# Kernel tuning notes

Measured on AMD Instinct MI355X. Metric: run time of the kernel, lower is better.

Reference implementation:

```python
import jax, jax.numpy as jnp
import numpy as np

B, H, S, DK = 2, 16, 2048, 64
P_DROP = 0.5
MASK_NEG = 1e9


def setup_inputs() -> dict:
    key = jax.random.key(0)
    kq, kk, kv = jax.random.split(key, 3)
    Q = jax.random.normal(kq, (B, H, S, DK), dtype=jnp.float32)
    K = jax.random.normal(kk, (B, H, S, DK), dtype=jnp.float32)
    V = jax.random.normal(kv, (B, H, S, DK), dtype=jnp.float32)
    attn_mask = jnp.ones((B, 1, S, S), dtype=jnp.float32)  # 1 = attend, 0 = masked
    return {"Q": Q, "K": K, "V": V, "attn_mask": attn_mask}


def reference(Q, K, V, attn_mask):
    # scores = Q @ K^T / sqrt(d_k)
    scores = jnp.einsum('bhqd,bhkd->bhqk', Q, K) / np.float32(np.sqrt(DK))
    # additive mask: (mask - 1) * 1e9
    scores = scores + (attn_mask - 1.0) * MASK_NEG
    attn = jax.nn.softmax(scores, axis=-1)
    # dropout p=0.5 (training mode in the torch module); deterministic key for reproducibility
    keep = jax.random.bernoulli(jax.random.key(42), 1.0 - P_DROP, attn.shape)
    attn_dropped = jnp.where(keep, attn / (1.0 - P_DROP), 0.0)
    context = jnp.einsum('bhqk,bhkd->bhqd', attn_dropped, V)
    return context, attn
```

## Files before the change

kernel.cpp:

```cpp
#include <hip/hip_runtime.h>
#include <stdint.h>

#define B_ 2
#define H_ 16
#define S_ 2048
#define D_ 64

__device__ __forceinline__ unsigned tf_keep(unsigned idx) {
  const unsigned k0 = 0u, k1 = 42u;
  const unsigned ks2 = k0 ^ k1 ^ 0x1BD11BDAu;
  unsigned x0 = k0;
  unsigned x1 = idx + k1;
#define ROTL(v, r) (((v) << (r)) | ((v) >> (32 - (r))))
#define RND(r) { x0 += x1; x1 = ROTL(x1, r); x1 ^= x0; }
  RND(13) RND(15) RND(26) RND(6)
  x0 += k1;  x1 += ks2 + 1u;
  RND(17) RND(29) RND(16) RND(24)
  x0 += ks2; x1 += k0 + 2u;
  RND(13) RND(15) RND(26) RND(6)
  x0 += k0;  x1 += k1 + 3u;
  RND(17) RND(29) RND(16) RND(24)
  x0 += k1;  x1 += ks2 + 4u;
  RND(13) RND(15) RND(26) RND(6)
  x0 += ks2; x1 += k0 + 5u;
#undef RND
#undef ROTL
  return ((x0 ^ x1) >> 31) ^ 1u;
}

extern "C" __global__ void __launch_bounds__(256, 2)
k1_scores(const float* __restrict__ Q, const float* __restrict__ K,
          const float* __restrict__ mask, float* __restrict__ E,
          float* __restrict__ inv_sums) {
  __shared__ float Qs[D_][16];
  __shared__ float Ks[D_][128];
  const int tid = threadIdx.x;
  const int w = tid >> 6, lane = tid & 63;
  const int qt = blockIdx.x & 127, bh = blockIdx.x >> 7, b = bh >> 4;
  const int q0 = qt << 4;

  const float* Qb = Q + ((size_t)bh * S_ + q0) * D_;
  const float* Kb = K + (size_t)bh * S_ * D_;
  const float* Mb = mask + ((size_t)b * S_ + q0) * S_;
  float* Eb = E + ((size_t)bh * S_ + q0) * S_;

  {
    const int ql = tid >> 4, d4 = tid & 15;
    const float4 v = *(const float4*)(Qb + ql * D_ + (d4 << 2));
    Qs[(d4 << 2) + 0][ql] = v.x;
    Qs[(d4 << 2) + 1][ql] = v.y;
    Qs[(d4 << 2) + 2][ql] = v.z;
    Qs[(d4 << 2) + 3][ql] = v.w;
  }

  float row_sum[4] = {0.0f, 0.0f, 0.0f, 0.0f};

  for (int kt = 0; kt < 16; ++kt) {
    __syncthreads();
#pragma unroll
    for (int rep = 0; rep < 8; ++rep) {
      const int item = (rep << 8) + tid;
      const int kl = item & 127, d4 = item >> 7;
      const float4 v = *(const float4*)(Kb + ((size_t)(kt << 7) + kl) * D_ + (d4 << 2));
      Ks[(d4 << 2) + 0][kl] = v.x;
      Ks[(d4 << 2) + 1][kl] = v.y;
      Ks[(d4 << 2) + 2][kl] = v.z;
      Ks[(d4 << 2) + 3][kl] = v.w;
    }
    __syncthreads();

    float sA[4] = {0.f, 0.f, 0.f, 0.f}, sB[4] = {0.f, 0.f, 0.f, 0.f};
#pragma unroll 16
    for (int d = 0; d < D_; ++d) {
      const float4 qv = *(const float4*)&Qs[d][w << 2];
      const float2 kv = *(const float2*)&Ks[d][lane << 1];
      const float qa[4] = {qv.x, qv.y, qv.z, qv.w};
#pragma unroll
      for (int i = 0; i < 4; ++i) {
        sA[i] += qa[i] * kv.x;
        sB[i] += qa[i] * kv.y;
      }
    }

    const int kc = (kt << 7) + (lane << 1);
#pragma unroll
    for (int i = 0; i < 4; ++i) {
      const int row = (w << 2) + i;
      const float2 mv = *(const float2*)(Mb + (size_t)row * S_ + kc);
      const float ex = __expf(sA[i] * 0.125f + (mv.x - 1.0f) * 1e9f);
      const float ey = __expf(sB[i] * 0.125f + (mv.y - 1.0f) * 1e9f);
      row_sum[i] += ex + ey;
      *(float2*)(Eb + (size_t)row * S_ + kc) = make_float2(ex, ey);
    }
  }

#pragma unroll
  for (int i = 0; i < 4; ++i) {
    float v = row_sum[i];
#pragma unroll
    for (int off = 32; off >= 1; off >>= 1) v += __shfl_xor(v, off, 64);
    row_sum[i] = v;
  }
  if (lane < 4) {
    float v = row_sum[0];
    if (lane == 1) v = row_sum[1];
    else if (lane == 2) v = row_sum[2];
    else if (lane == 3) v = row_sum[3];
    inv_sums[(size_t)bh * S_ + q0 + (w << 2) + lane] = 1.0f / v;
  }
}

extern "C" __global__ void __launch_bounds__(256, 2)
k2_pv(const float* __restrict__ V, const float* __restrict__ inv_sums,
      float* __restrict__ E ,
      float* __restrict__ ctx) {
  __shared__ float Vs[64][64];
  __shared__ float Ps[64][68];
  __shared__ float invs[64];
  const int tid = threadIdx.x;
  const int dg = tid & 15, qg = tid >> 4;
  const int qt = blockIdx.x & 31, bh = blockIdx.x >> 5;
  const int q0 = qt << 6;

  const float* Vb = V + (size_t)bh * S_ * D_;
  float* Eb = E + ((size_t)bh * S_ + q0) * S_;

  if (tid < 64) invs[tid] = inv_sums[(size_t)bh * S_ + q0 + tid];

  float acc[4][4];
#pragma unroll
  for (int i = 0; i < 4; ++i)
#pragma unroll
    for (int m = 0; m < 4; ++m) acc[i][m] = 0.0f;

  const unsigned rowbase = (unsigned)bh * S_ + (unsigned)q0;

  for (int kt = 0; kt < 32; ++kt) {
    __syncthreads();
#pragma unroll
    for (int rep = 0; rep < 4; ++rep) {
      const int idx = (rep << 8) + tid;
      const int d4 = idx & 15, kk = idx >> 4;
      const float4 v = *(const float4*)(Vb + ((size_t)(kt << 6) + kk) * D_ + (d4 << 2));
      *(float4*)&Vs[kk][d4 << 2] = v;
    }
#pragma unroll
    for (int rep = 0; rep < 4; ++rep) {
      const int idx = (rep << 8) + tid;
      const int k4 = idx & 15, ql = idx >> 4;
      float* ep = Eb + (size_t)ql * S_ + (kt << 6) + (k4 << 2);
      const float4 e = *(const float4*)ep;
      const float inv = invs[ql];
      const float4 an = make_float4(e.x * inv, e.y * inv, e.z * inv, e.w * inv);
      *(float4*)ep = an;
      const unsigned fb = ((rowbase + (unsigned)ql) << 11) +
                          (unsigned)((kt << 6) + (k4 << 2));
      Ps[(k4 << 2) + 0][ql] = tf_keep(fb + 0u) ? an.x * 2.0f : 0.0f;
      Ps[(k4 << 2) + 1][ql] = tf_keep(fb + 1u) ? an.y * 2.0f : 0.0f;
      Ps[(k4 << 2) + 2][ql] = tf_keep(fb + 2u) ? an.z * 2.0f : 0.0f;
      Ps[(k4 << 2) + 3][ql] = tf_keep(fb + 3u) ? an.w * 2.0f : 0.0f;
    }
    __syncthreads();
#pragma unroll 8
    for (int kk = 0; kk < 64; ++kk) {
      const float4 pq = *(const float4*)&Ps[kk][qg << 2];
      const float4 vv = *(const float4*)&Vs[kk][dg << 2];
      acc[0][0] += pq.x * vv.x; acc[0][1] += pq.x * vv.y; acc[0][2] += pq.x * vv.z; acc[0][3] += pq.x * vv.w;
      acc[1][0] += pq.y * vv.x; acc[1][1] += pq.y * vv.y; acc[1][2] += pq.y * vv.z; acc[1][3] += pq.y * vv.w;
      acc[2][0] += pq.z * vv.x; acc[2][1] += pq.z * vv.y; acc[2][2] += pq.z * vv.z; acc[2][3] += pq.z * vv.w;
      acc[3][0] += pq.w * vv.x; acc[3][1] += pq.w * vv.y; acc[3][2] += pq.w * vv.z; acc[3][3] += pq.w * vv.w;
    }
  }

  float* cb = ctx + ((size_t)bh * S_ + q0 + (qg << 2)) * D_ + (dg << 2);
#pragma unroll
  for (int i = 0; i < 4; ++i) {
    const float4 o = make_float4(acc[i][0], acc[i][1], acc[i][2], acc[i][3]);
    *(float4*)(cb + (size_t)i * D_) = o;
  }
}

extern "C" void kernel_launch(void* const* d_in, const int* in_sizes, int n_in,
                              void* d_out, int out_size, void* d_ws, size_t ws_size,
                              hipStream_t stream) {
  (void)in_sizes; (void)n_in; (void)out_size; (void)ws_size;
  const float* Q = (const float*)d_in[0];
  const float* K = (const float*)d_in[1];
  const float* V = (const float*)d_in[2];
  const float* mask = (const float*)d_in[3];
  float* ctx = (float*)d_out;
  float* attn = ctx + (size_t)B_ * H_ * S_ * D_;
  float* inv_sums = (float*)d_ws;

  hipLaunchKernelGGL(k1_scores, dim3(B_ * H_ * (S_ / 16)), dim3(256), 0, stream,
                     Q, K, mask, attn, inv_sums);
  hipLaunchKernelGGL(k2_pv, dim3(B_ * H_ * (S_ / 64)), dim3(256), 0, stream,
                     V, inv_sums, attn, ctx);
}
```

Measured before the change: 1.351 ms.

## Fuse score, softmax and PV kernels with bf16 exp cache in LDS

Replaces the two-kernel pipeline with a single fused kernel. Each block of 32 queries computes the exponentiated scores and keeps them in shared memory as bf16, computes the dropout-masked P·V product on the fly, and writes normalized attn once at the end. This removes the global round trip of the unnormalized exp matrix (one write, one read and one rewrite) and the second launch. The cost is large LDS usage (about 128KB for the bf16 cache), which limits occupancy, plus bf16 rounding of attn and of the P used for the context, which risks tolerance failures.

Measured after the change: 2.147 ms. +58.8%, slower.

```diff
diff --git a/kernel.cpp b/kernel.cpp
--- a/kernel.cpp
+++ b/kernel.cpp
@@ -5,6 +5,9 @@
 #define H_ 16
 #define S_ 2048
 #define D_ 64
+#define QT 32
+#define KT 64
+#define NKT (S_ / KT)
 
 __device__ __forceinline__ unsigned tf_keep(unsigned idx) {
   const unsigned k0 = 0u, k1 = 42u;
@@ -28,172 +31,203 @@
   return ((x0 ^ x1) >> 31) ^ 1u;
 }
 
-extern "C" __global__ void __launch_bounds__(256, 2)
-k1_scores(const float* __restrict__ Q, const float* __restrict__ K,
-          const float* __restrict__ mask, float* __restrict__ E,
-          float* __restrict__ inv_sums) {
-  __shared__ float Qs[D_][16];
-  __shared__ float Ks[D_][128];
+__device__ __forceinline__ unsigned short bf16_rne(float f) {
+  unsigned u = __float_as_uint(f);
+  u += 0x7fffu + ((u >> 16) & 1u);
+  return (unsigned short)(u >> 16);
+}
+
+__device__ __forceinline__ void unpk(unsigned u, float& lo, float& hi) {
+  lo = __uint_as_float(u << 16);
+  hi = __uint_as_float(u & 0xffff0000u);
+}
+
+extern "C" __global__ void __launch_bounds__(512, 2)
+fused_attn(const float* __restrict__ Q, const float* __restrict__ K,
+           const float* __restrict__ V, const float* __restrict__ mask,
+           float* __restrict__ ctx, float* __restrict__ attn) {
+  __shared__ __align__(16) float Qs[QT][68];
+  __shared__ __align__(16) float KVs[KT][64];
+  __shared__ __align__(16) unsigned short Es[QT][S_];
+  __shared__ __align__(16) unsigned short Pd[QT][72];
+  __shared__ float invs[QT];
+
   const int tid = threadIdx.x;
   const int w = tid >> 6, lane = tid & 63;
-  const int qt = blockIdx.x & 127, bh = blockIdx.x >> 7, b = bh >> 4;
-  const int q0 = qt << 4;
+  const int qt = blockIdx.x & 63;
+  const int bh = blockIdx.x >> 6;
+  const int b = bh >> 4;
+  const int q0 = qt << 5;
 
   const float* Qb = Q + ((size_t)bh * S_ + q0) * D_;
   const float* Kb = K + (size_t)bh * S_ * D_;
+  const float* Vb = V + (size_t)bh * S_ * D_;
   const float* Mb = mask + ((size_t)b * S_ + q0) * S_;
-  float* Eb = E + ((size_t)bh * S_ + q0) * S_;
+  const unsigned rowbase = (unsigned)(bh * S_ + q0);
 
   {
-    const int ql = tid >> 4, d4 = tid & 15;
-    const float4 v = *(const float4*)(Qb + ql * D_ + (d4 << 2));
-    Qs[(d4 << 2) + 0][ql] = v.x;
-    Qs[(d4 << 2) + 1][ql] = v.y;
-    Qs[(d4 << 2) + 2][ql] = v.z;
-    Qs[(d4 << 2) + 3][ql] = v.w;
-  }
-
-  float row_sum[4] = {0.0f, 0.0f, 0.0f, 0.0f};
-
-  for (int kt = 0; kt < 16; ++kt) {
-    __syncthreads();
-#pragma unroll
-    for (int rep = 0; rep < 8; ++rep) {
-      const int item = (rep << 8) + tid;
-      const int kl = item & 127, d4 = item >> 7;
-      const float4 v = *(const float4*)(Kb + ((size_t)(kt << 7) + kl) * D_ + (d4 << 2));
-      Ks[(d4 << 2) + 0][kl] = v.x;
-      Ks[(d4 << 2) + 1][kl] = v.y;
-      Ks[(d4 << 2) + 2][kl] = v.z;
-      Ks[(d4 << 2) + 3][kl] = v.w;
-    }
-    __syncthreads();
-
-    float sA[4] = {0.f, 0.f, 0.f, 0.f}, sB[4] = {0.f, 0.f, 0.f, 0.f};
-#pragma unroll 16
-    for (int d = 0; d < D_; ++d) {
-      const float4 qv = *(const float4*)&Qs[d][w << 2];
-      const float2 kv = *(const float2*)&Ks[d][lane << 1];
-      const float qa[4] = {qv.x, qv.y, qv.z, qv.w};
-#pragma unroll
-      for (int i = 0; i < 4; ++i) {
-        sA[i] += qa[i] * kv.x;
-        sB[i] += qa[i] * kv.y;
-      }
-    }
-
-    const int kc = (kt << 7) + (lane << 1);
+    const int qr = tid >> 4, d4 = tid & 15;
+    const float4 v = *(const float4*)(Qb + (size_t)qr * D_ + (d4 << 2));
+    *(float4*)&Qs[qr][d4 << 2] = v;
+  }
+
+  const int ksp = tid >> 8;
+  const int t8 = tid & 255;
+  const int qg2 = t8 >> 4;
+  const int dg = t8 & 15;
+
+  float rsum[4] = {0.f, 0.f, 0.f, 0.f};
+  float aA[4] = {0.f, 0.f, 0.f, 0.f};
+  float aB[4] = {0.f, 0.f, 0.f, 0.f};
+
+  const int ksw = lane & 15;
+  const float4* krow = (const float4*)&KVs[lane][0];
+
+#pragma unroll 1
+  for (int kt = 0; kt < NKT; ++kt) {
+    __syncthreads();
+#pragma unroll
+    for (int rep = 0; rep < 2; ++rep) {
+      const int f4 = (rep << 9) + tid;
+      const int kr = f4 >> 4, d4 = f4 & 15;
+      const float4 v = *(const float4*)(Kb + (size_t)((kt << 6) + kr) * D_ + (d4 << 2));
+      *(float4*)&KVs[kr][(d4 ^ (kr & 15)) << 2] = v;
+    }
+    __syncthreads();
+
+    const int kg = (kt << 6) + lane;
+    float mv0 = Mb[(size_t)((w << 2) + 0) * S_ + kg];
+    float mv1 = Mb[(size_t)((w << 2) + 1) * S_ + kg];
+    float mv2 = Mb[(size_t)((w << 2) + 2) * S_ + kg];
+    float mv3 = Mb[(size_t)((w << 2) + 3) * S_ + kg];
+
+    float s0 = 0.f, s1 = 0.f, s2 = 0.f, s3 = 0.f;
+#pragma unroll
+    for (int d4 = 0; d4 < 16; ++d4) {
+      const float4 kv = krow[d4 ^ ksw];
+      const float4 q0v = *(const float4*)&Qs[(w << 2) + 0][d4 << 2];
+      const float4 q1v = *(const float4*)&Qs[(w << 2) + 1][d4 << 2];
+      const float4 q2v = *(const float4*)&Qs[(w << 2) + 2][d4 << 2];
+      const float4 q3v = *(const float4*)&Qs[(w << 2) + 3][d4 << 2];
+      s0 = fmaf(q0v.x, kv.x, s0); s0 = fmaf(q0v.y, kv.y, s0);
+      s0 = fmaf(q0v.z, kv.z, s0); s0 = fmaf(q0v.w, kv.w, s0);
+      s1 = fmaf(q1v.x, kv.x, s1); s1 = fmaf(q1v.y, kv.y, s1);
+      s1 = fmaf(q1v.z, kv.z, s1); s1 = fmaf(q1v.w, kv.w, s1);
+      s2 = fmaf(q2v.x, kv.x, s2); s2 = fmaf(q2v.y, kv.y, s2);
+      s2 = fmaf(q2v.z, kv.z, s2); s2 = fmaf(q2v.w, kv.w, s2);
+      s3 = fmaf(q3v.x, kv.x, s3); s3 = fmaf(q3v.y, kv.y, s3);
+      s3 = fmaf(q3v.z, kv.z, s3); s3 = fmaf(q3v.w, kv.w, s3);
+    }
+
+    const float sc[4] = {s0, s1, s2, s3};
+    const float mm[4] = {mv0, mv1, mv2, mv3};
 #pragma unroll
     for (int i = 0; i < 4; ++i) {
       const int row = (w << 2) + i;
-      const float2 mv = *(const float2*)(Mb + (size_t)row * S_ + kc);
-      const float ex = __expf(sA[i] * 0.125f + (mv.x - 1.0f) * 1e9f);
-      const float ey = __expf(sB[i] * 0.125f + (mv.y - 1.0f) * 1e9f);
-      row_sum[i] += ex + ey;
-      *(float2*)(Eb + (size_t)row * S_ + kc) = make_float2(ex, ey);
-    }
-  }
+      const float e = __expf(sc[i] * 0.125f + (mm[i] - 1.0f) * 1e9f);
+      rsum[i] += e;
+      const unsigned short ebs = bf16_rne(e);
+      Es[row][kg] = ebs;
+      const unsigned idx = ((rowbase + (unsigned)row) << 11) + (unsigned)kg;
+      Pd[row][lane] = tf_keep(idx) ? ebs : (unsigned short)0;
+    }
+
+    __syncthreads();
+#pragma unroll
+    for (int rep = 0; rep < 2; ++rep) {
+      const int f4 = (rep << 9) + tid;
+      const int kr = f4 >> 4, d4 = f4 & 15;
+      const float4 v = *(const float4*)(Vb + (size_t)((kt << 6) + kr) * D_ + (d4 << 2));
+      *(float4*)&KVs[kr][d4 << 2] = v;
+    }
+    __syncthreads();
+
+#pragma unroll
+    for (int k8 = 0; k8 < 4; ++k8) {
+      const int k0l = (ksp << 5) + (k8 << 3);
+      const uint4 pa4 = *(const uint4*)&Pd[(qg2 << 1) + 0][k0l];
+      const uint4 pb4 = *(const uint4*)&Pd[(qg2 << 1) + 1][k0l];
+      float pA[8], pB[8];
+      unpk(pa4.x, pA[0], pA[1]); unpk(pa4.y, pA[2], pA[3]);
+      unpk(pa4.z, pA[4], pA[5]); unpk(pa4.w, pA[6], pA[7]);
+      unpk(pb4.x, pB[0], pB[1]); unpk(pb4.y, pB[2], pB[3]);
+      unpk(pb4.z, pB[4], pB[5]); unpk(pb4.w, pB[6], pB[7]);
+#pragma unroll
+      for (int j = 0; j < 8; ++j) {
+        const float4 vv = *(const float4*)&KVs[k0l + j][dg << 2];
+        aA[0] = fmaf(pA[j], vv.x, aA[0]); aA[1] = fmaf(pA[j], vv.y, aA[1]);
+        aA[2] = fmaf(pA[j], vv.z, aA[2]); aA[3] = fmaf(pA[j], vv.w, aA[3]);
+        aB[0] = fmaf(pB[j], vv.x, aB[0]); aB[1] = fmaf(pB[j], vv.y, aB[1]);
+        aB[2] = fmaf(pB[j], vv.z, aB[2]); aB[3] = fmaf(pB[j], vv.w, aB[3]);
+      }
+    }
+  }
+
+  __syncthreads();
 
 #pragma unroll
   for (int i = 0; i < 4; ++i) {
-    float v = row_sum[i];
+    float v = rsum[i];
 #pragma unroll
     for (int off = 32; off >= 1; off >>= 1) v += __shfl_xor(v, off, 64);
-    row_sum[i] = v;
+    rsum[i] = v;
   }
   if (lane < 4) {
-    float v = row_sum[0];
-    if (lane == 1) v = row_sum[1];
-    else if (lane == 2) v = row_sum[2];
-    else if (lane == 3) v = row_sum[3];
-    inv_sums[(size_t)bh * S_ + q0 + (w << 2) + lane] = 1.0f / v;
-  }
-}
-
-extern "C" __global__ void __launch_bounds__(256, 2)
-k2_pv(const float* __restrict__ V, const float* __restrict__ inv_sums,
-      float* __restrict__ E ,
-      float* __restrict__ ctx) {
-  __shared__ float Vs[64][64];
-  __shared__ float Ps[64][68];
-  __shared__ float invs[64];
-  const int tid = threadIdx.x;
-  const int dg = tid & 15, qg = tid >> 4;
-  const int qt = blockIdx.x & 31, bh = blockIdx.x >> 5;
-  const int q0 = qt << 6;
-
-  const float* Vb = V + (size_t)bh * S_ * D_;
-  float* Eb = E + ((size_t)bh * S_ + q0) * S_;
-
-  if (tid < 64) invs[tid] = inv_sums[(size_t)bh * S_ + q0 + tid];
-
-  float acc[4][4];
-#pragma unroll
-  for (int i = 0; i < 4; ++i)
-#pragma unroll
-    for (int m = 0; m < 4; ++m) acc[i][m] = 0.0f;
-
-  const unsigned rowbase = (unsigned)bh * S_ + (unsigned)q0;
-
-  for (int kt = 0; kt < 32; ++kt) {
-    __syncthreads();
-#pragma unroll
-    for (int rep = 0; rep < 4; ++rep) {
-      const int idx = (rep << 8) + tid;
-      const int d4 = idx & 15, kk = idx >> 4;
-      const float4 v = *(const float4*)(Vb + ((size_t)(kt << 6) + kk) * D_ + (d4 << 2));
-      *(float4*)&Vs[kk][d4 << 2] = v;
-    }
-#pragma unroll
-    for (int rep = 0; rep < 4; ++rep) {
-      const int idx = (rep << 8) + tid;
-      const int k4 = idx & 15, ql = idx >> 4;
-      float* ep = Eb + (size_t)ql * S_ + (kt << 6) + (k4 << 2);
-      const float4 e = *(const float4*)ep;
-      const float inv = invs[ql];
-      const float4 an = make_float4(e.x * inv, e.y * inv, e.z * inv, e.w * inv);
-      *(float4*)ep = an;
-      const unsigned fb = ((rowbase + (unsigned)ql) << 11) +
-                          (unsigned)((kt << 6) + (k4 << 2));
-      Ps[(k4 << 2) + 0][ql] = tf_keep(fb + 0u) ? an.x * 2.0f : 0.0f;
-      Ps[(k4 << 2) + 1][ql] = tf_keep(fb + 1u) ? an.y * 2.0f : 0.0f;
-      Ps[(k4 << 2) + 2][ql] = tf_keep(fb + 2u) ? an.z * 2.0f : 0.0f;
-      Ps[(k4 << 2) + 3][ql] = tf_keep(fb + 3u) ? an.w * 2.0f : 0.0f;
-    }
-    __syncthreads();
-#pragma unroll 8
-    for (int kk = 0; kk < 64; ++kk) {
-      const float4 pq = *(const float4*)&Ps[kk][qg << 2];
-      const float4 vv = *(const float4*)&Vs[kk][dg << 2];
-      acc[0][0] += pq.x * vv.x; acc[0][1] += pq.x * vv.y; acc[0][2] += pq.x * vv.z; acc[0][3] += pq.x * vv.w;
-      acc[1][0] += pq.y * vv.x; acc[1][1] += pq.y * vv.y; acc[1][2] += pq.y * vv.z; acc[1][3] += pq.y * vv.w;
-      acc[2][0] += pq.z * vv.x; acc[2][1] += pq.z * vv.y; acc[2][2] += pq.z * vv.z; acc[2][3] += pq.z * vv.w;
-      acc[3][0] += pq.w * vv.x; acc[3][1] += pq.w * vv.y; acc[3][2] += pq.w * vv.z; acc[3][3] += pq.w * vv.w;
-    }
-  }
-
-  float* cb = ctx + ((size_t)bh * S_ + q0 + (qg << 2)) * D_ + (dg << 2);
-#pragma unroll
-  for (int i = 0; i < 4; ++i) {
-    const float4 o = make_float4(acc[i][0], acc[i][1], acc[i][2], acc[i][3]);
-    *(float4*)(cb + (size_t)i * D_) = o;
+    float v = rsum[0];
+    if (lane == 1) v = rsum[1];
+    else if (lane == 2) v = rsum[2];
+    else if (lane == 3) v = rsum[3];
+    invs[(w << 2) + lane] = 1.0f / v;
+  }
+
+  float* red = &KVs[0][0];
+  if (ksp) {
+    *(float4*)&red[((qg2 << 1) + 0) * 64 + (dg << 2)] = make_float4(aA[0], aA[1], aA[2], aA[3]);
+    *(float4*)&red[((qg2 << 1) + 1) * 64 + (dg << 2)] = make_float4(aB[0], aB[1], aB[2], aB[3]);
+  }
+  __syncthreads();
+
+  if (!ksp) {
+    const float4 rA = *(const float4*)&red[((qg2 << 1) + 0) * 64 + (dg << 2)];
+    const float4 rB = *(const float4*)&red[((qg2 << 1) + 1) * 64 + (dg << 2)];
+    const float iA = invs[(qg2 << 1) + 0] * 2.0f;
+    const float iB = invs[(qg2 << 1) + 1] * 2.0f;
+    float* cb = ctx + ((size_t)bh * S_ + q0) * D_;
+    const float4 oA = make_float4((aA[0] + rA.x) * iA, (aA[1] + rA.y) * iA,
+                                  (aA[2] + rA.z) * iA, (aA[3] + rA.w) * iA);
+    const float4 oB = make_float4((aB[0] + rB.x) * iB, (aB[1] + rB.y) * iB,
+                                  (aB[2] + rB.z) * iB, (aB[3] + rB.w) * iB);
+    *(float4*)(cb + (size_t)((qg2 << 1) + 0) * D_ + (dg << 2)) = oA;
+    *(float4*)(cb + (size_t)((qg2 << 1) + 1) * D_ + (dg << 2)) = oB;
+  }
+
+  float* Ab = attn + ((size_t)bh * S_ + q0) * S_;
+#pragma unroll
+  for (int rep = 0; rep < 16; ++rep) {
+    const int g = (rep << 9) + tid;
+    const int row = g >> 8, c8 = g & 255;
+    const uint4 ev = *(const uint4*)&Es[row][c8 << 3];
+    const float inv = invs[row];
+    float o0, o1, o2, o3, o4, o5, o6, o7;
+    unpk(ev.x, o0, o1); unpk(ev.y, o2, o3);
+    unpk(ev.z, o4, o5); unpk(ev.w, o6, o7);
+    float* ap = Ab + (size_t)row * S_ + (c8 << 3);
+    *(float4*)ap = make_float4(o0 * inv, o1 * inv, o2 * inv, o3 * inv);
+    *(float4*)(ap + 4) = make_float4(o4 * inv, o5 * inv, o6 * inv, o7 * inv);
   }
 }
 
 extern "C" void kernel_launch(void* const* d_in, const int* in_sizes, int n_in,
                               void* d_out, int out_size, void* d_ws, size_t ws_size,
                               hipStream_t stream) {
-  (void)in_sizes; (void)n_in; (void)out_size; (void)ws_size;
+  (void)in_sizes; (void)n_in; (void)out_size; (void)d_ws; (void)ws_size;
   const float* Q = (const float*)d_in[0];
   const float* K = (const float*)d_in[1];
   const float* V = (const float*)d_in[2];
   const float* mask = (const float*)d_in[3];
   float* ctx = (float*)d_out;
   float* attn = ctx + (size_t)B_ * H_ * S_ * D_;
-  float* inv_sums = (float*)d_ws;
-
-  hipLaunchKernelGGL(k1_scores, dim3(B_ * H_ * (S_ / 16)), dim3(256), 0, stream,
-                     Q, K, mask, attn, inv_sums);
-  hipLaunchKernelGGL(k2_pv, dim3(B_ * H_ * (S_ / 64)), dim3(256), 0, stream,
-                     V, inv_sums, attn, ctx);
-}
+
+  hipLaunchKernelGGL(fused_attn, dim3(B_ * H_ * (S_ / QT)), dim3(512), 0, stream,
+                     Q, K, V, mask, ctx, attn);
+}
```
